# Kernel tuning notes

Hardware: AMD Instinct MI355X
Metric: run time of the kernel (lower is better)

## Reference

```python
import jax, jax.numpy as jnp
import numpy as np

N_NODES = 50000
N_EDGES = 800000
N_GRAPHS = 64
IN_DIM = 128
HID = 128
S, C = 4, 16
DIM1 = 3 * S * S  # 48
OUT_DIM = DIM1 * C  # 768


def gcn_conv(x, W, b, src, dst, w):
    """PyG GCNConv: linear transform, then sym-normalized aggregation with self-loops (weight 1)."""
    n = x.shape[0]
    h = x @ W  # [N, out]
    deg = jnp.zeros((n,), x.dtype).at[dst].add(w) + 1.0  # self-loop weight 1
    dinv = jax.lax.rsqrt(deg)
    norm = dinv[src] * w * dinv[dst]  # [E]
    agg = jnp.zeros_like(h).at[dst].add(h[src] * norm[:, None])
    agg = agg + h * (1.0 / deg)[:, None]  # self-loop messages
    return agg + b


def setup_inputs() -> dict:
    key = jax.random.key(0)
    ks = jax.random.split(key, 16)
    x = jax.random.normal(ks[0], (N_NODES, IN_DIM), jnp.float32)
    edge_index = jax.random.randint(ks[1], (2, N_EDGES), 0, N_NODES, jnp.int64)
    edge_attr = jax.random.uniform(ks[2], (N_EDGES,), jnp.float32)
    batch = jnp.sort(jax.random.randint(ks[3], (N_NODES,), 0, N_GRAPHS, jnp.int64))

    def glorot(k, fan_in, fan_out):
        s = np.sqrt(6.0 / (fan_in + fan_out)).astype(np.float32)
        return jax.random.uniform(k, (fan_in, fan_out), jnp.float32, -s, s)

    return {
        "x": x, "edge_index": edge_index, "edge_attr": edge_attr, "batch": batch,
        "W1": glorot(ks[4], IN_DIM, HID), "b1": jnp.zeros((HID,), jnp.float32),
        "W2": glorot(ks[5], HID, HID // 2), "b2": jnp.zeros((HID // 2,), jnp.float32),
        "W3": glorot(ks[6], HID // 2, HID // 4), "b3": jnp.zeros((HID // 4,), jnp.float32),
        "Wl": glorot(ks[7], HID // 4, OUT_DIM), "bl": jnp.zeros((OUT_DIM,), jnp.float32),
    }


def reference(x, edge_index, edge_attr, batch, W1, b1, W2, b2, W3, b3, Wl, bl):
    src, dst = edge_index[0], edge_index[1]
    w = edge_attr / edge_attr.max()
    h = jax.nn.relu(gcn_conv(x, W1, b1, src, dst, w))
    h = jax.nn.relu(gcn_conv(h, W2, b2, src, dst, w))
    h = jax.nn.relu(gcn_conv(h, W3, b3, src, dst, w))
    # global mean pool over graphs
    sums = jax.ops.segment_sum(h, batch, num_segments=N_GRAPHS)
    cnt = jax.ops.segment_sum(jnp.ones((h.shape[0],), h.dtype), batch, num_segments=N_GRAPHS)
    pooled = sums / jnp.maximum(cnt, 1.0)[:, None]
    out = pooled @ Wl + bl  # [G, OUT_DIM]
    return out.reshape(N_GRAPHS, DIM1, C)
```

## Files before the change

kernel.cpp:

```cpp
#include <hip/hip_runtime.h>
#include <hip/hip_bf16.h>

#define NN 50000
#define NE 800000
#define NG 64
#define OUTD 768

#define G1B ((NN + 63) / 64)
#define MAXB 128
#define SSEG 32
#define TTL 4
#define ESEG (NE / SSEG)
#define NTL (NN / TTL)
#define HRB (SSEG * TTL)

__device__ __forceinline__ float bflo(unsigned int u) { return __uint_as_float(u << 16); }
__device__ __forceinline__ float bfhi(unsigned int u) { return __uint_as_float(u & 0xffff0000u); }
__device__ __forceinline__ unsigned short f2bf(float f) {
    unsigned int u = __float_as_uint(f);
    return (unsigned short)((u + 0x7fffu + ((u >> 16) & 1u)) >> 16);
}
__device__ __forceinline__ unsigned int pack2bf(float lo, float hi) {
    return (unsigned int)f2bf(lo) | ((unsigned int)f2bf(hi) << 16);
}

typedef __attribute__((ext_vector_type(8))) short bf16x8;
typedef __attribute__((ext_vector_type(4))) float f32x4;
union FragU { uint4 u4; bf16x8 v; };

template <int K, int N>
constexpr int mfma_lds_bytes() { return (K / 32) * (N / 16) * 1024; }

template <int K, int N, typename TX>
__device__ __forceinline__ void mfma_gemm_body(char* smem,
                                               const TX* __restrict__ X,
                                               const float* __restrict__ W,
                                               unsigned short* __restrict__ Y,
                                               int nRows, int bx) {
    constexpr int NCT = N / 16;
    constexpr int KS = K / 32;
    const int tid = threadIdx.x;

    for (int q = tid; q < KS * NCT * 64; q += 256) {
        int lane = q & 63;
        int fi = q >> 6;
        int ct = fi % NCT, kc = fi / NCT;
        int col = ct * 16 + (lane & 15);
        int kb = kc * 32 + ((lane >> 4) << 3);
        uint4 w;
        w.x = pack2bf(W[(size_t)(kb + 0) * N + col], W[(size_t)(kb + 1) * N + col]);
        w.y = pack2bf(W[(size_t)(kb + 2) * N + col], W[(size_t)(kb + 3) * N + col]);
        w.z = pack2bf(W[(size_t)(kb + 4) * N + col], W[(size_t)(kb + 5) * N + col]);
        w.w = pack2bf(W[(size_t)(kb + 6) * N + col], W[(size_t)(kb + 7) * N + col]);
        *(uint4*)(smem + (size_t)q * 16) = w;
    }
    __syncthreads();

    const int lane = tid & 63;
    const int wv = tid >> 6;
    const int m = lane & 15;
    const int quad = lane >> 4;
    const int row = bx * 64 + wv * 16 + m;
    const bool rowok = row < nRows;
    const TX* xr = X + (size_t)(rowok ? row : 0) * K;

    f32x4 acc[NCT];
#pragma unroll
    for (int ct = 0; ct < NCT; ++ct) acc[ct] = (f32x4){0.f, 0.f, 0.f, 0.f};

#pragma unroll
    for (int kc = 0; kc < KS; ++kc) {
        const int k0 = kc * 32 + quad * 8;
        FragU a;
        if constexpr (sizeof(TX) == 4) {
            float4 a0 = make_float4(0.f, 0.f, 0.f, 0.f), a1 = a0;
            if (rowok) {
                a0 = *(const float4*)(xr + k0);
                a1 = *(const float4*)(xr + k0 + 4);
            }
            a.u4 = make_uint4(pack2bf(a0.x, a0.y), pack2bf(a0.z, a0.w),
                              pack2bf(a1.x, a1.y), pack2bf(a1.z, a1.w));
        } else {
            a.u4 = rowok ? *(const uint4*)(xr + k0) : make_uint4(0, 0, 0, 0);
        }
#pragma unroll
        for (int ct = 0; ct < NCT; ++ct) {
            FragU b;
            b.u4 = *(const uint4*)(smem + ((size_t)(kc * NCT + ct) * 64 + lane) * 16);
            acc[ct] = __builtin_amdgcn_mfma_f32_16x16x32_bf16(a.v, b.v, acc[ct], 0, 0, 0);
        }
    }

    const int orowb = bx * 64 + wv * 16 + quad * 4;
#pragma unroll
    for (int ct = 0; ct < NCT; ++ct) {
        int col = ct * 16 + m;
#pragma unroll
        for (int r = 0; r < 4; ++r) {
            int orow = orowb + r;
            if (orow < nRows) Y[(size_t)orow * N + col] = f2bf(acc[ct][r]);
        }
    }
}

template <int K, int N, typename TX>
__global__ __launch_bounds__(256) void mfma_gemm_kernel(const TX* __restrict__ X,
                                                        const float* __restrict__ W,
                                                        unsigned short* __restrict__ Y,
                                                        int nRows) {
    extern __shared__ char smem[];
    mfma_gemm_body<K, N>(smem, X, W, Y, nRows, blockIdx.x);
}

__global__ __launch_bounds__(256) void fused1_kernel(const float* __restrict__ x,
                                                     const float* __restrict__ W1,
                                                     unsigned short* __restrict__ bufA,
                                                     const float* __restrict__ ea,
                                                     unsigned int* wmax,
                                                     const int* __restrict__ dst,
                                                     int* __restrict__ rank,
                                                     unsigned short* __restrict__ pcnt) {
    extern __shared__ char smem[];
    const int b = blockIdx.x;
    if (b < G1B) {
        mfma_gemm_body<128, 128>(smem, x, W1, bufA, NN, b);
    } else if (b < G1B + MAXB) {
        float* red = (float*)smem;
        const int bb = b - G1B;
        const float4* ea4 = (const float4*)ea;
        float m = 0.0f;
        for (int i = bb * 256 + threadIdx.x; i < NE / 4; i += MAXB * 256) {
            float4 v = ea4[i];
            m = fmaxf(fmaxf(m, fmaxf(v.x, v.y)), fmaxf(v.z, v.w));
        }
        red[threadIdx.x] = m;
        __syncthreads();
        for (int off = 128; off > 0; off >>= 1) {
            if (threadIdx.x < off)
                red[threadIdx.x] = fmaxf(red[threadIdx.x], red[threadIdx.x + off]);
            __syncthreads();
        }
        if (threadIdx.x == 0) atomicMax(wmax, __float_as_uint(red[0]));
    } else {
        const int b2 = b - G1B - MAXB;
        const int seg = b2 >> 2;
        const int tile = b2 & 3;
        unsigned int* lcnt = (unsigned int*)smem;
        for (int i = threadIdx.x; i < NTL / 2; i += 256) lcnt[i] = 0;
        __syncthreads();
        const int base = seg * ESEG;
        const int nlo = tile * NTL;
        const int4* dst4 = (const int4*)(dst + base);
        for (int g = threadIdx.x; g < ESEG / 4; g += 256) {
            const int4 v = dst4[g];
            const int e0 = base + g * 4;
            const int dd[4] = {v.x, v.y, v.z, v.w};
#pragma unroll
            for (int j = 0; j < 4; ++j) {
                int d = dd[j] - nlo;
                if ((unsigned)d < (unsigned)NTL) {
                    unsigned sh = (unsigned)(d & 1) << 4;
                    unsigned old = atomicAdd(&lcnt[d >> 1], 1u << sh);
                    rank[e0 + j] = (int)((old >> sh) & 0xffffu);
                }
            }
        }
        __syncthreads();
        unsigned int* prow32 = (unsigned int*)(pcnt + (size_t)seg * NN + nlo);
        for (int i = threadIdx.x; i < NTL / 2; i += 256) prow32[i] = lcnt[i];
    }
}

__global__ __launch_bounds__(256) void comb_kernel(unsigned short* __restrict__ pcnt,
                                                   int* __restrict__ hist,
                                                   int* __restrict__ blocksum) {
    __shared__ int red[256];
    int n = blockIdx.x * 256 + threadIdx.x;
    int run = 0;
    if (n < NN) {
#pragma unroll
        for (int s = 0; s < SSEG; ++s) {
            size_t idx = (size_t)s * NN + n;
            int v = pcnt[idx];
            pcnt[idx] = (unsigned short)run;
            run += v;
        }
        hist[n] = run;
    }
    red[threadIdx.x] = (n < NN) ? run : 0;
    __syncthreads();
    for (int off = 128; off > 0; off >>= 1) {
        if (threadIdx.x < off) red[threadIdx.x] += red[threadIdx.x + off];
        __syncthreads();
    }
    if (threadIdx.x == 0) blocksum[blockIdx.x] = red[0];
}

__global__ __launch_bounds__(256) void scan3_kernel(const int* __restrict__ hist,
                                                    const int* __restrict__ blocksum,
                                                    int* __restrict__ rowptr, int n, int nb) {
    __shared__ int sb[256];
    __shared__ int s[256];
    const int tid = threadIdx.x;
    int bv = (tid < nb) ? blocksum[tid] : 0;
    sb[tid] = bv;
    __syncthreads();
    for (int off = 1; off < 256; off <<= 1) {
        int t = (tid >= off) ? sb[tid - off] : 0;
        __syncthreads();
        sb[tid] += t;
        __syncthreads();
    }
    const int boff = (blockIdx.x > 0) ? sb[blockIdx.x - 1] : 0;
    const int total = sb[nb - 1];

    int i = blockIdx.x * 256 + tid;
    int v = (i < n) ? hist[i] : 0;
    s[tid] = v;
    __syncthreads();
    for (int off = 1; off < 256; off <<= 1) {
        int t = (tid >= off) ? s[tid - off] : 0;
        __syncthreads();
        s[tid] += t;
        __syncthreads();
    }
    if (i < n) rowptr[i] = boff + s[tid] - v;
    if (blockIdx.x == 0 && tid == 0) rowptr[n] = total;
}

__global__ void scat_kernel(const int* __restrict__ src, const int* __restrict__ dst,
                            const float* __restrict__ ea,
                            const int* __restrict__ rowptr,
                            const unsigned short* __restrict__ pcnt,
                            const int* __restrict__ rank,
                            int2* __restrict__ epack, int nE4) {
    int g = blockIdx.x * blockDim.x + threadIdx.x;
    if (g >= nE4) return;
    const int s = (g * 4) / ESEG;
    const size_t pb = (size_t)s * NN;
    const int4 d4 = ((const int4*)dst)[g];
    const int4 s4 = ((const int4*)src)[g];
    const float4 e4 = ((const float4*)ea)[g];
    const int4 r4 = ((const int4*)rank)[g];
    const int dd[4] = {d4.x, d4.y, d4.z, d4.w};
    const int ss[4] = {s4.x, s4.y, s4.z, s4.w};
    const float ee[4] = {e4.x, e4.y, e4.z, e4.w};
    const int rr[4] = {r4.x, r4.y, r4.z, r4.w};
#pragma unroll
    for (int j = 0; j < 4; ++j) {
        int pos = rowptr[dd[j]] + (int)pcnt[pb + dd[j]] + rr[j];
        epack[pos] = make_int2(ss[j], __float_as_int(ee[j]));
    }
}

__global__ void deg_kernel(const int2* __restrict__ epack, const int* __restrict__ rowptr,
                           const unsigned int* __restrict__ wmax,
                           float* __restrict__ nrm, float* __restrict__ invdeg,
                           float* __restrict__ selfc, int n) {
    int i = blockIdx.x * blockDim.x + threadIdx.x;
    if (i >= n) return;
    float rw = 1.0f / __uint_as_float(*wmax);
    float srw = sqrtf(rw);
    int s0 = rowptr[i], s1 = rowptr[i + 1];
    float sa = 0.f, sb = 0.f;
    int e = s0;
    for (; e + 2 <= s1; e += 2) {
        sa += __int_as_float(epack[e].y);
        sb += __int_as_float(epack[e + 1].y);
    }
    if (e < s1) sa += __int_as_float(epack[e].y);
    float d = fmaf(sa + sb, rw, 1.0f);
    float rs = rsqrtf(d);
    nrm[i] = rs * srw;
    invdeg[i] = 1.0f / d;
    selfc[i] = rs / srw;
}

template <int D, int MODE>
__global__ __launch_bounds__(256) void agg_kernel(const unsigned short* __restrict__ H,
                                                  const int* __restrict__ rowptr,
                                                  const int2* __restrict__ epack,
                                                  const float* __restrict__ nrm,
                                                  const float* __restrict__ invdeg,
                                                  const float* __restrict__ selfc,
                                                  const float* __restrict__ bias,
                                                  unsigned short* __restrict__ out,
                                                  int nNodes) {
    constexpr int LPE = D / 8;
    constexpr int EPW = 64 / LPE;
    const int lane = threadIdx.x & 63;
    const int n = (blockIdx.x << 2) | (threadIdx.x >> 6);
    if (n >= nNodes) return;
    const int esub = lane / LPE;
    const int f8 = (lane % LPE) * 8;
    const int s0 = rowptr[n];
    const int cnt = rowptr[n + 1] - s0;
    const int2* ep = epack + s0;

    float a[8] = {};
#define AGG8(c_, u_)                                                            \
    a[0] = fmaf(c_, bflo(u_.x), a[0]); a[1] = fmaf(c_, bfhi(u_.x), a[1]);       \
    a[2] = fmaf(c_, bflo(u_.y), a[2]); a[3] = fmaf(c_, bfhi(u_.y), a[3]);       \
    a[4] = fmaf(c_, bflo(u_.z), a[4]); a[5] = fmaf(c_, bfhi(u_.z), a[5]);       \
    a[6] = fmaf(c_, bflo(u_.w), a[6]); a[7] = fmaf(c_, bfhi(u_.w), a[7]);
#define COEF(p_) (MODE == 0 ? nrm[p_.x] * __int_as_float(p_.y) : __int_as_float(p_.y))

    int kb = 0;
    for (; kb + 4 * EPW <= cnt; kb += 4 * EPW) {
        const int2 p0 = ep[kb + 0 * EPW + esub];
        const int2 p1 = ep[kb + 1 * EPW + esub];
        const int2 p2 = ep[kb + 2 * EPW + esub];
        const int2 p3 = ep[kb + 3 * EPW + esub];
        const uint4 u0 = *(const uint4*)(H + (size_t)p0.x * D + f8);
        const uint4 u1 = *(const uint4*)(H + (size_t)p1.x * D + f8);
        const uint4 u2 = *(const uint4*)(H + (size_t)p2.x * D + f8);
        const uint4 u3 = *(const uint4*)(H + (size_t)p3.x * D + f8);
        const float c0 = COEF(p0);
        const float c1 = COEF(p1);
        const float c2 = COEF(p2);
        const float c3 = COEF(p3);
        AGG8(c0, u0) AGG8(c1, u1) AGG8(c2, u2) AGG8(c3, u3)
    }
    for (; kb + 2 * EPW <= cnt; kb += 2 * EPW) {
        const int2 p0 = ep[kb + esub];
        const int2 p1 = ep[kb + EPW + esub];
        const uint4 u0 = *(const uint4*)(H + (size_t)p0.x * D + f8);
        const uint4 u1 = *(const uint4*)(H + (size_t)p1.x * D + f8);
        const float c0 = COEF(p0);
        const float c1 = COEF(p1);
        AGG8(c0, u0) AGG8(c1, u1)
    }
    for (; kb < cnt; kb += EPW) {
        const int idx = kb + esub;
        const bool ok = idx < cnt;
        const int2 p = ok ? ep[idx] : make_int2(n, 0);
        const uint4 u = *(const uint4*)(H + (size_t)p.x * D + f8);
        const float c = ok ? COEF(p) : 0.f;
        AGG8(c, u)
    }
#undef COEF
#undef AGG8
#pragma unroll
    for (int off = LPE; off < 64; off <<= 1) {
#pragma unroll
        for (int j = 0; j < 8; ++j) a[j] += __shfl_xor(a[j], off);
    }
    if (esub == 0) {
        const float dn = nrm[n];
        const float sc = (MODE == 0) ? invdeg[n] : selfc[n];
        const uint4 un = *(const uint4*)(H + (size_t)n * D + f8);
        const float4 b0 = *(const float4*)(bias + f8);
        const float4 b1 = *(const float4*)(bias + f8 + 4);
        float o[8];
        o[0] = fmaxf(fmaf(dn, a[0], fmaf(sc, bflo(un.x), b0.x)), 0.f);
        o[1] = fmaxf(fmaf(dn, a[1], fmaf(sc, bfhi(un.x), b0.y)), 0.f);
        o[2] = fmaxf(fmaf(dn, a[2], fmaf(sc, bflo(un.y), b0.z)), 0.f);
        o[3] = fmaxf(fmaf(dn, a[3], fmaf(sc, bfhi(un.y), b0.w)), 0.f);
        o[4] = fmaxf(fmaf(dn, a[4], fmaf(sc, bflo(un.z), b1.x)), 0.f);
        o[5] = fmaxf(fmaf(dn, a[5], fmaf(sc, bfhi(un.z), b1.y)), 0.f);
        o[6] = fmaxf(fmaf(dn, a[6], fmaf(sc, bflo(un.w), b1.z)), 0.f);
        o[7] = fmaxf(fmaf(dn, a[7], fmaf(sc, bfhi(un.w), b1.w)), 0.f);
        if constexpr (MODE != 2) {
#pragma unroll
            for (int j = 0; j < 8; ++j) o[j] *= dn;
        }
        uint4 w;
        w.x = pack2bf(o[0], o[1]);
        w.y = pack2bf(o[2], o[3]);
        w.z = pack2bf(o[4], o[5]);
        w.w = pack2bf(o[6], o[7]);
        *(uint4*)(out + (size_t)n * D + f8) = w;
    }
}

__global__ __launch_bounds__(1024) void poolfin_kernel(const unsigned short* __restrict__ h,
                                                       const int* __restrict__ batch,
                                                       const float* __restrict__ Wl,
                                                       const float* __restrict__ bl,
                                                       float* __restrict__ out, int n) {
    const int g = blockIdx.x;
    int lo = 0, hi = n;
    while (lo < hi) { int m = (lo + hi) >> 1; if (batch[m] < g) lo = m + 1; else hi = m; }
    const int start = lo;
    lo = start; hi = n;
    while (lo < hi) { int m = (lo + hi) >> 1; if (batch[m] < g + 1) lo = m + 1; else hi = m; }
    const int end = lo;

    __shared__ float part[1024];
    __shared__ float spool[32];
    const int f = threadIdx.x & 31;
    const int r = threadIdx.x >> 5;
    float acc = 0.f;
    for (int i = start + r; i < end; i += 32)
        acc += __uint_as_float((unsigned int)h[(size_t)i * 32 + f] << 16);
    part[threadIdx.x] = acc;
    __syncthreads();
    if (threadIdx.x < 32) {
        float s = 0.f;
#pragma unroll
        for (int q = 0; q < 32; ++q) s += part[q * 32 + f];
        float inv = 1.0f / fmaxf((float)(end - start), 1.0f);
        spool[f] = s * inv;
    }
    __syncthreads();
    if (threadIdx.x < OUTD) {
        const int o = threadIdx.x;
        float a2 = bl[o];
#pragma unroll
        for (int k = 0; k < 32; ++k)
            a2 = fmaf(spool[k], Wl[k * OUTD + o], a2);
        out[(size_t)g * OUTD + o] = a2;
    }
}

extern "C" void kernel_launch(void* const* d_in, const int* in_sizes, int n_in,
                              void* d_out, int out_size, void* d_ws, size_t ws_size,
                              hipStream_t stream) {
    const float* x = (const float*)d_in[0];
    const int* eidx = (const int*)d_in[1];
    const float* ea = (const float*)d_in[2];
    const int* batch = (const int*)d_in[3];
    const float* W1 = (const float*)d_in[4];
    const float* b1 = (const float*)d_in[5];
    const float* W2 = (const float*)d_in[6];
    const float* b2 = (const float*)d_in[7];
    const float* W3 = (const float*)d_in[8];
    const float* b3 = (const float*)d_in[9];
    const float* Wl = (const float*)d_in[10];
    const float* bl = (const float*)d_in[11];
    const int* src = eidx;
    const int* dst = eidx + NE;

    char* p = (char*)d_ws;
    auto take = [&](size_t bytes) {
        char* r = p;
        p += (bytes + 255) & ~(size_t)255;
        return r;
    };
    float* nrm = (float*)take(NN * 4);
    float* invdeg = (float*)take(NN * 4);
    float* selfc = (float*)take(NN * 4);
    int* hist = (int*)take(NN * 4);
    int* rowptr = (int*)take((NN + 1) * 4);
    int* blocksum = (int*)take(256 * 4);
    int2* epack = (int2*)take((size_t)NE * 8);
    unsigned int* wmax = (unsigned int*)take(4);
    unsigned short* bufA = (unsigned short*)take((size_t)NN * 128 * 2);
    unsigned short* bufB = (unsigned short*)take((size_t)NN * 128 * 2);
    int* rank = (int*)bufB;
    unsigned short* pcnt = (unsigned short*)((char*)bufB + (size_t)NE * 4 + 256);

    const int nblk = (NN + 255) / 256;
    const int e4blk = (NE / 4 + 255) / 256;

    hipMemsetAsync(wmax, 0, 4, stream);

    constexpr int LDS1 = mfma_lds_bytes<128, 128>();
    static_assert(LDS1 >= NTL * 2, "HR branch LDS (packed u16 counters) must fit");
    fused1_kernel<<<G1B + MAXB + HRB, 256, LDS1, stream>>>(x, W1, bufA, ea, wmax,
                                                           dst, rank, pcnt);
    comb_kernel<<<nblk, 256, 0, stream>>>(pcnt, hist, blocksum);
    scan3_kernel<<<nblk, 256, 0, stream>>>(hist, blocksum, rowptr, NN, nblk);
    scat_kernel<<<e4blk, 256, 0, stream>>>(src, dst, ea, rowptr, pcnt, rank, epack, NE / 4);
    deg_kernel<<<nblk, 256, 0, stream>>>(epack, rowptr, wmax, nrm, invdeg, selfc, NN);

    agg_kernel<128, 0><<<(NN + 3) / 4, 256, 0, stream>>>(bufA, rowptr, epack, nrm,
                                                         invdeg, selfc, b1, bufB, NN);
    mfma_gemm_kernel<128, 64, unsigned short>
        <<<G1B, 256, mfma_lds_bytes<128, 64>(), stream>>>(bufB, W2, bufA, NN);
    agg_kernel<64, 1><<<(NN + 3) / 4, 256, 0, stream>>>(bufA, rowptr, epack, nrm,
                                                        invdeg, selfc, b2, bufB, NN);
    mfma_gemm_kernel<64, 32, unsigned short>
        <<<G1B, 256, mfma_lds_bytes<64, 32>(), stream>>>(bufB, W3, bufA, NN);
    agg_kernel<32, 2><<<(NN + 3) / 4, 256, 0, stream>>>(bufA, rowptr, epack, nrm,
                                                        invdeg, selfc, b3, bufB, NN);

    poolfin_kernel<<<NG, 1024, 0, stream>>>(bufB, batch, Wl, bl, (float*)d_out, NN);
}
```

Measured before the change: 255.0 us.

## Fuse CSR build stages into one kernel with software grid barriers

Merges the comb, scan, scatter and degree kernels into the first fused kernel. The 256 non-GEMM blocks synchronise among themselves through atomic-counter grid barriers, which removes four kernel launches and their gaps. This relies on all CHB blocks being co-resident alongside the GEMM blocks (launch bounds 256,5) or the barrier will deadlock. Scatter work is now spread over only 256 blocks in a grid-stride loop rather than a full grid.

```diff
diff --git a/kernel.cpp b/kernel.cpp
--- a/kernel.cpp
+++ b/kernel.cpp
@@ -13,6 +13,8 @@
 #define ESEG (NE / SSEG)
 #define NTL (NN / TTL)
 #define HRB (SSEG * TTL)
+#define CHB (MAXB + HRB)
+#define NBLK ((NN + 255) / 256)
 
 __device__ __forceinline__ float bflo(unsigned int u) { return __uint_as_float(u << 16); }
 __device__ __forceinline__ float bfhi(unsigned int u) { return __uint_as_float(u & 0xffff0000u); }
@@ -112,46 +114,51 @@
     mfma_gemm_body<K, N>(smem, X, W, Y, nRows, blockIdx.x);
 }
 
-__global__ __launch_bounds__(256) void fused1_kernel(const float* __restrict__ x,
-                                                     const float* __restrict__ W1,
-                                                     unsigned short* __restrict__ bufA,
-                                                     const float* __restrict__ ea,
-                                                     unsigned int* wmax,
-                                                     const int* __restrict__ dst,
-                                                     int* __restrict__ rank,
-                                                     unsigned short* __restrict__ pcnt) {
+__global__ __launch_bounds__(256, 5) void build_kernel(
+        const float* __restrict__ x, const float* __restrict__ W1,
+        unsigned short* __restrict__ bufA,
+        const float* __restrict__ ea, unsigned int* wmax,
+        const int* __restrict__ src, const int* __restrict__ dst,
+        int* __restrict__ rank, unsigned short* __restrict__ pcnt,
+        int* __restrict__ blocksum, int* __restrict__ rowptr,
+        int2* __restrict__ epack,
+        float* __restrict__ nrm, float* __restrict__ invdeg,
+        float* __restrict__ selfc, unsigned int* syncc) {
     extern __shared__ char smem[];
     const int b = blockIdx.x;
+    const int tid = threadIdx.x;
     if (b < G1B) {
         mfma_gemm_body<128, 128>(smem, x, W1, bufA, NN, b);
-    } else if (b < G1B + MAXB) {
+        return;
+    }
+    const int cb = b - G1B;
+
+    if (cb < MAXB) {
         float* red = (float*)smem;
-        const int bb = b - G1B;
         const float4* ea4 = (const float4*)ea;
         float m = 0.0f;
-        for (int i = bb * 256 + threadIdx.x; i < NE / 4; i += MAXB * 256) {
+        for (int i = cb * 256 + tid; i < NE / 4; i += MAXB * 256) {
             float4 v = ea4[i];
             m = fmaxf(fmaxf(m, fmaxf(v.x, v.y)), fmaxf(v.z, v.w));
         }
-        red[threadIdx.x] = m;
+        red[tid] = m;
         __syncthreads();
         for (int off = 128; off > 0; off >>= 1) {
-            if (threadIdx.x < off)
-                red[threadIdx.x] = fmaxf(red[threadIdx.x], red[threadIdx.x + off]);
+            if (tid < off) red[tid] = fmaxf(red[tid], red[tid + off]);
             __syncthreads();
         }
-        if (threadIdx.x == 0) atomicMax(wmax, __float_as_uint(red[0]));
+        if (tid == 0) atomicMax(wmax, __float_as_uint(red[0]));
     } else {
-        const int b2 = b - G1B - MAXB;
+        const int b2 = cb - MAXB;
         const int seg = b2 >> 2;
         const int tile = b2 & 3;
         unsigned int* lcnt = (unsigned int*)smem;
-        for (int i = threadIdx.x; i < NTL / 2; i += 256) lcnt[i] = 0;
+        for (int i = tid; i < NTL / 2; i += 256) lcnt[i] = 0;
         __syncthreads();
         const int base = seg * ESEG;
         const int nlo = tile * NTL;
         const int4* dst4 = (const int4*)(dst + base);
-        for (int g = threadIdx.x; g < ESEG / 4; g += 256) {
+        for (int g = tid; g < ESEG / 4; g += 256) {
             const int4 v = dst4[g];
             const int e0 = base + g * 4;
             const int dd[4] = {v.x, v.y, v.z, v.w};
@@ -167,113 +174,106 @@
         }
         __syncthreads();
         unsigned int* prow32 = (unsigned int*)(pcnt + (size_t)seg * NN + nlo);
-        for (int i = threadIdx.x; i < NTL / 2; i += 256) prow32[i] = lcnt[i];
-    }
-}
-
-__global__ __launch_bounds__(256) void comb_kernel(unsigned short* __restrict__ pcnt,
-                                                   int* __restrict__ hist,
-                                                   int* __restrict__ blocksum) {
-    __shared__ int red[256];
-    int n = blockIdx.x * 256 + threadIdx.x;
+        for (int i = tid; i < NTL / 2; i += 256) prow32[i] = lcnt[i];
+    }
+
+    auto gbar = [&](int k) {
+        __syncthreads();
+        if (tid == 0) {
+            __threadfence();
+            atomicAdd(&syncc[k], 1u);
+            while (atomicAdd(&syncc[k], 0u) < (unsigned)CHB)
+                __builtin_amdgcn_s_sleep(2);
+            __threadfence();
+        }
+        __syncthreads();
+    };
+
+    gbar(0);
+
+    int* sc = (int*)smem;
+    int* sb = (int*)smem + 256;
+    const int n = cb * 256 + tid;
     int run = 0;
-    if (n < NN) {
-#pragma unroll
-        for (int s = 0; s < SSEG; ++s) {
-            size_t idx = (size_t)s * NN + n;
-            int v = pcnt[idx];
-            pcnt[idx] = (unsigned short)run;
-            run += v;
-        }
-        hist[n] = run;
-    }
-    red[threadIdx.x] = (n < NN) ? run : 0;
-    __syncthreads();
-    for (int off = 128; off > 0; off >>= 1) {
-        if (threadIdx.x < off) red[threadIdx.x] += red[threadIdx.x + off];
-        __syncthreads();
-    }
-    if (threadIdx.x == 0) blocksum[blockIdx.x] = red[0];
-}
-
-__global__ __launch_bounds__(256) void scan3_kernel(const int* __restrict__ hist,
-                                                    const int* __restrict__ blocksum,
-                                                    int* __restrict__ rowptr, int n, int nb) {
-    __shared__ int sb[256];
-    __shared__ int s[256];
-    const int tid = threadIdx.x;
-    int bv = (tid < nb) ? blocksum[tid] : 0;
-    sb[tid] = bv;
-    __syncthreads();
-    for (int off = 1; off < 256; off <<= 1) {
-        int t = (tid >= off) ? sb[tid - off] : 0;
-        __syncthreads();
-        sb[tid] += t;
-        __syncthreads();
-    }
-    const int boff = (blockIdx.x > 0) ? sb[blockIdx.x - 1] : 0;
-    const int total = sb[nb - 1];
-
-    int i = blockIdx.x * 256 + tid;
-    int v = (i < n) ? hist[i] : 0;
-    s[tid] = v;
-    __syncthreads();
-    for (int off = 1; off < 256; off <<= 1) {
-        int t = (tid >= off) ? s[tid - off] : 0;
-        __syncthreads();
-        s[tid] += t;
-        __syncthreads();
-    }
-    if (i < n) rowptr[i] = boff + s[tid] - v;
-    if (blockIdx.x == 0 && tid == 0) rowptr[n] = total;
-}
-
-__global__ void scat_kernel(const int* __restrict__ src, const int* __restrict__ dst,
-                            const float* __restrict__ ea,
-                            const int* __restrict__ rowptr,
-                            const unsigned short* __restrict__ pcnt,
-                            const int* __restrict__ rank,
-                            int2* __restrict__ epack, int nE4) {
-    int g = blockIdx.x * blockDim.x + threadIdx.x;
-    if (g >= nE4) return;
-    const int s = (g * 4) / ESEG;
-    const size_t pb = (size_t)s * NN;
-    const int4 d4 = ((const int4*)dst)[g];
-    const int4 s4 = ((const int4*)src)[g];
-    const float4 e4 = ((const float4*)ea)[g];
-    const int4 r4 = ((const int4*)rank)[g];
-    const int dd[4] = {d4.x, d4.y, d4.z, d4.w};
-    const int ss[4] = {s4.x, s4.y, s4.z, s4.w};
-    const float ee[4] = {e4.x, e4.y, e4.z, e4.w};
-    const int rr[4] = {r4.x, r4.y, r4.z, r4.w};
-#pragma unroll
-    for (int j = 0; j < 4; ++j) {
-        int pos = rowptr[dd[j]] + (int)pcnt[pb + dd[j]] + rr[j];
-        epack[pos] = make_int2(ss[j], __float_as_int(ee[j]));
-    }
-}
-
-__global__ void deg_kernel(const int2* __restrict__ epack, const int* __restrict__ rowptr,
-                           const unsigned int* __restrict__ wmax,
-                           float* __restrict__ nrm, float* __restrict__ invdeg,
-                           float* __restrict__ selfc, int n) {
-    int i = blockIdx.x * blockDim.x + threadIdx.x;
-    if (i >= n) return;
-    float rw = 1.0f / __uint_as_float(*wmax);
-    float srw = sqrtf(rw);
-    int s0 = rowptr[i], s1 = rowptr[i + 1];
-    float sa = 0.f, sb = 0.f;
-    int e = s0;
-    for (; e + 2 <= s1; e += 2) {
-        sa += __int_as_float(epack[e].y);
-        sb += __int_as_float(epack[e + 1].y);
-    }
-    if (e < s1) sa += __int_as_float(epack[e].y);
-    float d = fmaf(sa + sb, rw, 1.0f);
-    float rs = rsqrtf(d);
-    nrm[i] = rs * srw;
-    invdeg[i] = 1.0f / d;
-    selfc[i] = rs / srw;
+    if (cb < NBLK) {
+        if (n < NN) {
+#pragma unroll
+            for (int s = 0; s < SSEG; ++s) {
+                size_t idx = (size_t)s * NN + n;
+                int v = pcnt[idx];
+                pcnt[idx] = (unsigned short)run;
+                run += v;
+            }
+        }
+        sc[tid] = run;
+        __syncthreads();
+        for (int off = 1; off < 256; off <<= 1) {
+            int t = (tid >= off) ? sc[tid - off] : 0;
+            __syncthreads();
+            sc[tid] += t;
+            __syncthreads();
+        }
+        if (tid == 0) atomicExch(&blocksum[cb], sc[255]);
+    }
+    gbar(1);
+
+    if (cb < NBLK) {
+        int bv = (tid < NBLK) ? atomicAdd(&blocksum[tid], 0) : 0;
+        sb[tid] = bv;
+        __syncthreads();
+        for (int off = 1; off < 256; off <<= 1) {
+            int t = (tid >= off) ? sb[tid - off] : 0;
+            __syncthreads();
+            sb[tid] += t;
+            __syncthreads();
+        }
+        const int boff = (cb > 0) ? sb[cb - 1] : 0;
+        if (n < NN) rowptr[n] = boff + sc[tid] - run;
+        if (cb == NBLK - 1 && tid == 0) rowptr[NN] = sb[NBLK - 1];
+    }
+    gbar(2);
+
+    for (int g = cb * 256 + tid; g < NE / 4; g += CHB * 256) {
+        const int s = (g * 4) / ESEG;
+        const size_t pb = (size_t)s * NN;
+        const int4 d4 = ((const int4*)dst)[g];
+        const int4 s4 = ((const int4*)src)[g];
+        const float4 e4 = ((const float4*)ea)[g];
+        const int4 r4 = ((const int4*)rank)[g];
+        const int dd[4] = {d4.x, d4.y, d4.z, d4.w};
+        const int ss[4] = {s4.x, s4.y, s4.z, s4.w};
+        const float ee[4] = {e4.x, e4.y, e4.z, e4.w};
+        const int rr[4] = {r4.x, r4.y, r4.z, r4.w};
+#pragma unroll
+        for (int j = 0; j < 4; ++j) {
+            int pos = rowptr[dd[j]] + (int)pcnt[pb + dd[j]] + rr[j];
+            epack[pos] = make_int2(ss[j], __float_as_int(ee[j]));
+        }
+    }
+    gbar(3);
+
+    if (cb < NBLK) {
+        float* s_rw = (float*)smem + 512;
+        if (tid == 0) s_rw[0] = 1.0f / __uint_as_float(atomicAdd(wmax, 0u));
+        __syncthreads();
+        if (n < NN) {
+            float rw = s_rw[0];
+            float srw = sqrtf(rw);
+            int s0 = rowptr[n], s1 = rowptr[n + 1];
+            float sa = 0.f, sbv = 0.f;
+            int e = s0;
+            for (; e + 2 <= s1; e += 2) {
+                sa += __int_as_float(epack[e].y);
+                sbv += __int_as_float(epack[e + 1].y);
+            }
+            if (e < s1) sa += __int_as_float(epack[e].y);
+            float d = fmaf(sa + sbv, rw, 1.0f);
+            float rs = rsqrtf(d);
+            nrm[n] = rs * srw;
+            invdeg[n] = 1.0f / d;
+            selfc[n] = rs / srw;
+        }
+    }
 }
 
 template <int D, int MODE>
@@ -440,29 +440,24 @@
     float* nrm = (float*)take(NN * 4);
     float* invdeg = (float*)take(NN * 4);
     float* selfc = (float*)take(NN * 4);
-    int* hist = (int*)take(NN * 4);
     int* rowptr = (int*)take((NN + 1) * 4);
     int* blocksum = (int*)take(256 * 4);
     int2* epack = (int2*)take((size_t)NE * 8);
-    unsigned int* wmax = (unsigned int*)take(4);
+    unsigned int* wmax = (unsigned int*)take(32);
+    unsigned int* syncc = wmax + 1;
     unsigned short* bufA = (unsigned short*)take((size_t)NN * 128 * 2);
     unsigned short* bufB = (unsigned short*)take((size_t)NN * 128 * 2);
     int* rank = (int*)bufB;
     unsigned short* pcnt = (unsigned short*)((char*)bufB + (size_t)NE * 4 + 256);
 
-    const int nblk = (NN + 255) / 256;
-    const int e4blk = (NE / 4 + 255) / 256;
-
-    hipMemsetAsync(wmax, 0, 4, stream);
+    hipMemsetAsync(wmax, 0, 32, stream);
 
     constexpr int LDS1 = mfma_lds_bytes<128, 128>();
-    static_assert(LDS1 >= NTL * 2, "HR branch LDS (packed u16 counters) must fit");
-    fused1_kernel<<<G1B + MAXB + HRB, 256, LDS1, stream>>>(x, W1, bufA, ea, wmax,
-                                                           dst, rank, pcnt);
-    comb_kernel<<<nblk, 256, 0, stream>>>(pcnt, hist, blocksum);
-    scan3_kernel<<<nblk, 256, 0, stream>>>(hist, blocksum, rowptr, NN, nblk);
-    scat_kernel<<<e4blk, 256, 0, stream>>>(src, dst, ea, rowptr, pcnt, rank, epack, NE / 4);
-    deg_kernel<<<nblk, 256, 0, stream>>>(epack, rowptr, wmax, nrm, invdeg, selfc, NN);
+    static_assert(LDS1 >= NTL * 2, "HR phase LDS (packed u16 counters) must fit");
+    build_kernel<<<G1B + CHB, 256, LDS1, stream>>>(x, W1, bufA, ea, wmax,
+                                                   src, dst, rank, pcnt,
+                                                   blocksum, rowptr, epack,
+                                                   nrm, invdeg, selfc, syncc);
 
     agg_kernel<128, 0><<<(NN + 3) / 4, 256, 0, stream>>>(bufA, rowptr, epack, nrm,
                                                          invdeg, selfc, b1, bufB, NN);
```

Measured after the change: 350.9 us. 37.6% more time.
